# Performance work log

Measured on AMD Instinct MI355X. Metric: run time of the kernel, lower is better.

Reference implementation:

```python
import math
import jax, jax.numpy as jnp
import numpy as np

DIM = 192
HEADS = 6
WIN = (16, 16)
N = WIN[0] * WIN[1]
B_ = 256
NW = 64
CPB_HIDDEN = 512


def _relative_coords_table(window_size):
    Wh, Ww = window_size
    h = np.arange(-(Wh - 1), Wh, dtype=np.float32)
    w = np.arange(-(Ww - 1), Ww, dtype=np.float32)
    table = np.stack(np.meshgrid(h, w, indexing='ij'), axis=-1)[None]  # (1, 2Wh-1, 2Ww-1, 2)
    table[..., 0] /= (Wh - 1)
    table[..., 1] /= (Ww - 1)
    table *= 8.0
    table = np.sign(table) * np.log2(np.abs(table) + 1.0) / np.log2(8.0)
    return table.astype(np.float32)


def _relative_position_index(window_size):
    Wh, Ww = window_size
    coords = np.stack(np.meshgrid(np.arange(Wh), np.arange(Ww), indexing='ij'))  # (2, Wh, Ww)
    flat = coords.reshape(2, -1)
    rel = flat[:, :, None] - flat[:, None, :]  # (2, N, N)
    rel = rel.transpose(1, 2, 0).astype(np.int64)
    rel[..., 0] += Wh - 1
    rel[..., 1] += Ww - 1
    rel[..., 0] *= 2 * Ww - 1
    return rel.sum(-1)  # (N, N)


def setup_inputs() -> dict:
    key = jax.random.key(0)
    ks = jax.random.split(key, 9)
    s = 1.0 / math.sqrt(DIM)
    inp = {
        'x': jax.random.normal(ks[0], (B_, N, DIM), dtype=jnp.float32),
        'mask': jax.random.normal(ks[1], (NW, N, N), dtype=jnp.float32),
        'qkv_w': jax.random.normal(ks[2], (3 * DIM, DIM), dtype=jnp.float32) * s,
        'qkv_b': jnp.zeros((3 * DIM,), dtype=jnp.float32),
        'proj_w': jax.random.normal(ks[3], (DIM, DIM), dtype=jnp.float32) * s,
        'proj_b': jnp.zeros((DIM,), dtype=jnp.float32),
        'logit_scale': jnp.full((HEADS, 1, 1), math.log(10.0), dtype=jnp.float32),
        'cpb_w1': jax.random.normal(ks[4], (CPB_HIDDEN, 2), dtype=jnp.float32) * (1.0 / math.sqrt(2.0)),
        'cpb_b1': jnp.zeros((CPB_HIDDEN,), dtype=jnp.float32),
        'cpb_w2': jax.random.normal(ks[5], (HEADS, CPB_HIDDEN), dtype=jnp.float32) * (1.0 / math.sqrt(CPB_HIDDEN)),
        'coords_table': jnp.asarray(_relative_coords_table(WIN)),
        'rel_index': jnp.asarray(_relative_position_index(WIN)),
    }
    return inp


def reference(x, mask, qkv_w, qkv_b, proj_w, proj_b, logit_scale,
              cpb_w1, cpb_b1, cpb_w2, coords_table, rel_index):
    Bw, n, C = x.shape
    H = logit_scale.shape[0]
    Dh = C // H
    eps = 1e-12

    qkv = x @ qkv_w.T + qkv_b                             # (B_, N, 3C)
    qkv = qkv.reshape(Bw, n, 3, H, Dh).transpose(2, 0, 3, 1, 4)
    q, k, v = qkv[0], qkv[1], qkv[2]                      # (B_, H, N, Dh)

    qn = q / jnp.maximum(jnp.linalg.norm(q, axis=-1, keepdims=True), eps)
    kn = k / jnp.maximum(jnp.linalg.norm(k, axis=-1, keepdims=True), eps)
    attn = jnp.einsum('bhnd,bhmd->bhnm', qn, kn)

    scale = jnp.exp(jnp.minimum(logit_scale, math.log(1.0 / 0.01)))  # (H,1,1)
    attn = attn * scale[None]

    # CPB MLP bias: (1, 2Wh-1, 2Ww-1, 2) -> (-1, H), gather, sigmoid-scale
    hbt = jax.nn.relu(coords_table @ cpb_w1.T + cpb_b1) @ cpb_w2.T   # (1, 2Wh-1, 2Ww-1, H)
    bias_table = hbt.reshape(-1, H)
    bias = bias_table[rel_index.reshape(-1)].reshape(n, n, H).transpose(2, 0, 1)
    attn = attn + 16.0 * jax.nn.sigmoid(bias)[None]

    nW = mask.shape[0]
    attn = attn.reshape(Bw // nW, nW, H, n, n) + mask[None, :, None]
    attn = attn.reshape(Bw, H, n, n)

    attn = jax.nn.softmax(attn, axis=-1)
    out = jnp.einsum('bhnm,bhmd->bhnd', attn, v)
    out = out.transpose(0, 2, 1, 3).reshape(Bw, n, C)
    return out @ proj_w.T + proj_b
```

## Files before the change

### kernel.cpp

```cpp
#include <hip/hip_runtime.h>

using bf16 = __bf16;
typedef bf16 bf16x4 __attribute__((ext_vector_type(4)));
typedef bf16 bf16x8 __attribute__((ext_vector_type(8)));
typedef float f32x4 __attribute__((ext_vector_type(4)));

__device__ __forceinline__ int swz192(int row, int col) {
  return row * 192 + (col ^ ((row & 7) << 3));
}
__device__ __forceinline__ int qk_idx(int row, int col) {
  return (row >> 1) * 64 + (row & 1) * 32 + (col ^ (((row >> 1) & 3) << 3));
}
__device__ __forceinline__ int vt_idx(int d, int n) {
  return d * 256 + (((n + ((d >> 3) << 4)) & 255) ^ ((d & 7) << 3));
}
__device__ __forceinline__ int p_idx4(int wv, int r, int c) {
  return wv * 1024 + r * 64 + (c ^ ((r & 7) << 3));
}

#define LOG2E 1.44269504088896f
#define GLOAD_LDS(src, dst)                                                     \
  __builtin_amdgcn_global_load_lds(                                             \
      (const __attribute__((address_space(1))) void*)(src),                     \
      (__attribute__((address_space(3))) void*)(dst), 16, 0, 0)

template <bool OUT_F32, bool NORM_QK, int NT>
__global__ __launch_bounds__(256) void k_gemm(const bf16* __restrict__ A,
                                              const bf16* __restrict__ W,
                                              const float* __restrict__ bias,
                                              const float* __restrict__ lsc,
                                              void* __restrict__ Op, int Ntot) {
  __shared__ bf16 As[64 * 192];
  __shared__ bf16 Bs[64 * 192];
  const int bid = blockIdx.x;
  const int xcd = bid & 7;
  const int j = bid >> 3;
  const int m0 = (xcd + 8 * (j / NT)) * 64;
  const int n0 = (j % NT) * 64;
  const int t = threadIdx.x;

#pragma unroll
  for (int i = 0; i < 6; ++i) {
    const int f = t + i * 256;
    const int row = f / 24, c8 = f % 24;
    const int csw = (c8 ^ (row & 7)) * 8;
    GLOAD_LDS(&A[(m0 + row) * 192 + csw], &As[f * 8]);
    GLOAD_LDS(&W[(n0 + row) * 192 + csw], &Bs[f * 8]);
  }
  __syncthreads();

  const int w = t >> 6, lane = t & 63, lo = lane & 15, hi = lane >> 4;
  const int wm = (w >> 1) * 32, wn = (w & 1) * 32;
  f32x4 acc[2][2];
#pragma unroll
  for (int a = 0; a < 2; ++a)
#pragma unroll
    for (int c = 0; c < 2; ++c) acc[a][c] = f32x4{0.f, 0.f, 0.f, 0.f};

#pragma unroll
  for (int ks = 0; ks < 6; ++ks) {
    const int k0 = ks * 32 + hi * 8;
    bf16x8 af[2], bfr[2];
#pragma unroll
    for (int ri = 0; ri < 2; ++ri)
      af[ri] = *reinterpret_cast<const bf16x8*>(&As[swz192(wm + ri * 16 + lo, k0)]);
#pragma unroll
    for (int ci = 0; ci < 2; ++ci)
      bfr[ci] = *reinterpret_cast<const bf16x8*>(&Bs[swz192(wn + ci * 16 + lo, k0)]);
#pragma unroll
    for (int ri = 0; ri < 2; ++ri)
#pragma unroll
      for (int ci = 0; ci < 2; ++ci)
        acc[ri][ci] = __builtin_amdgcn_mfma_f32_16x16x32_bf16(af[ri], bfr[ci], acc[ri][ci], 0, 0, 0);
  }

  if (NORM_QK) {
    const int cb = n0 + wn;
    const bool donorm = (cb < 384);
    float smul = 1.f;
    if (cb < 192)
      smul = expf(fminf(lsc[cb >> 5], 4.605170185988091f)) * LOG2E;
    const int col0 = cb + lo;
    const float b0 = bias[col0], b1 = bias[col0 + 16];
    bf16* O = (bf16*)Op;
#pragma unroll
    for (int ri = 0; ri < 2; ++ri)
#pragma unroll
      for (int rr = 0; rr < 4; ++rr) {
        float v0 = acc[ri][0][rr] + b0;
        float v1 = acc[ri][1][rr] + b1;
        if (donorm) {
          float ss = v0 * v0 + v1 * v1;
          ss += __shfl_xor(ss, 1, 16);
          ss += __shfl_xor(ss, 2, 16);
          ss += __shfl_xor(ss, 4, 16);
          ss += __shfl_xor(ss, 8, 16);
          const float rn = smul / fmaxf(sqrtf(ss), 1e-12f);
          v0 *= rn;
          v1 *= rn;
        }
        const int row = m0 + wm + ri * 16 + hi * 4 + rr;
        O[row * Ntot + col0] = (bf16)v0;
        O[row * Ntot + col0 + 16] = (bf16)v1;
      }
  } else {
#pragma unroll
    for (int ri = 0; ri < 2; ++ri)
#pragma unroll
      for (int ci = 0; ci < 2; ++ci) {
        const int col = n0 + wn + ci * 16 + lo;
        const float bv = bias[col];
#pragma unroll
        for (int rr = 0; rr < 4; ++rr) {
          const int row = m0 + wm + ri * 16 + hi * 4 + rr;
          const float val = acc[ri][ci][rr] + bv;
          if (OUT_F32)
            __builtin_nontemporal_store(val, &((float*)Op)[row * Ntot + col]);
          else
            ((bf16*)Op)[row * Ntot + col] = (bf16)val;
        }
      }
  }
}

__global__ void k_cpb1(const float* __restrict__ ct, const float* __restrict__ w1,
                       const float* __restrict__ b1, const float* __restrict__ w2,
                       float* __restrict__ bt) {
  int idx = blockIdx.x * 256 + threadIdx.x;
  if (idx >= 961 * 6) return;
  int r = idx / 6, hh = idx % 6;
  float t0 = ct[r * 2], t1 = ct[r * 2 + 1];
  float acc = 0.f;
  for (int j = 0; j < 512; ++j) {
    float hv = fmaf(w1[j * 2], t0, fmaf(w1[j * 2 + 1], t1, b1[j]));
    hv = fmaxf(hv, 0.f);
    acc = fmaf(hv, w2[hh * 512 + j], acc);
  }
  bt[idx] = acc;
}

__global__ __launch_bounds__(256) void k_prep(
    const float* __restrict__ x, bf16* __restrict__ xb,
    const float* __restrict__ qkv_w, bf16* __restrict__ qkv_wb,
    const float* __restrict__ proj_w, bf16* __restrict__ proj_wb,
    const float* __restrict__ mask, bf16* __restrict__ maskT,
    const float* __restrict__ bt, const int* __restrict__ rel,
    float* __restrict__ biasfT) {
  __shared__ float tile[64][65];
  const int bid = blockIdx.x;
  if (bid < 6216) {
    const float* in;
    bf16* o;
    int vb;
    if (bid < 6144) { in = x; o = xb; vb = bid; }
    else if (bid < 6198) { in = qkv_w; o = qkv_wb; vb = bid - 6144; }
    else { in = proj_w; o = proj_wb; vb = bid - 6198; }
    const int i = (vb * 256 + threadIdx.x) * 8;
    const f32x4 a = *reinterpret_cast<const f32x4*>(&in[i]);
    const f32x4 b = *reinterpret_cast<const f32x4*>(&in[i + 4]);
    bf16x8 v;
    v[0] = (bf16)a[0]; v[1] = (bf16)a[1]; v[2] = (bf16)a[2]; v[3] = (bf16)a[3];
    v[4] = (bf16)b[0]; v[5] = (bf16)b[1]; v[6] = (bf16)b[2]; v[7] = (bf16)b[3];
    *reinterpret_cast<bf16x8*>(&o[i]) = v;
  } else if (bid < 7240) {
    const int rem = bid - 6216;
    const int mb = rem >> 4;
    const int it = (rem & 15) >> 2, jt = rem & 3;
    const int tx = threadIdx.x & 63, ty = threadIdx.x >> 6;
    const float* mp = mask + mb * 65536;
#pragma unroll
    for (int rr = 0; rr < 16; ++rr)
      tile[rr * 4 + ty][tx] = mp[(it * 64 + rr * 4 + ty) * 256 + jt * 64 + tx];
    __syncthreads();
    bf16* op = maskT + mb * 65536;
#pragma unroll
    for (int rr = 0; rr < 16; ++rr)
      op[(jt * 64 + rr * 4 + ty) * 256 + it * 64 + tx] = (bf16)(LOG2E * tile[tx][rr * 4 + ty]);
  } else {
    const int idx = (bid - 7240) * 256 + threadIdx.x;
    const int hh = idx >> 16;
    const int jj = (idx >> 8) & 255;
    const int i = idx & 255;
    const float v = bt[rel[i * 256 + jj] * 6 + hh];
    biasfT[idx] = LOG2E * 16.f / (1.f + __builtin_amdgcn_exp2f(-LOG2E * v));
  }
}

__global__ __launch_bounds__(256) void k_attn(const bf16* __restrict__ qkv,
                                              const bf16* __restrict__ maskT,
                                              const float* __restrict__ biasfT,
                                              bf16* __restrict__ aout) {
  __shared__ bf16 ksh[256 * 32];
  __shared__ bf16 vts[32 * 256];
  __shared__ bf16 ps[4 * 16 * 64];

  const int bid = blockIdx.x;
  const int x = bid & 7, i = bid >> 3;
  const int mb = x * 8 + i / 24;
  const int rem = i % 24;
  const int b = (rem / 6) * 64 + mb;
  const int h = rem % 6;
  const int t = threadIdx.x;

  const int rsub = t >> 2;
  const int c4s = t & 3;
#pragma unroll
  for (int p = 0; p < 4; ++p) {
    const int row = p * 64 + rsub;
    const int base = (b * 256 + row) * 576 + h * 32 + c4s * 8;
    *reinterpret_cast<bf16x8*>(&ksh[qk_idx(row, c4s * 8)]) =
        *reinterpret_cast<const bf16x8*>(&qkv[base + 192]);
    bf16x8 v = *reinterpret_cast<const bf16x8*>(&qkv[base + 384]);
#pragma unroll
    for (int jj = 0; jj < 8; ++jj) vts[vt_idx(c4s * 8 + jj, row)] = v[jj];
  }
  __syncthreads();

  const int w = t >> 6, lane = t & 63, lo = lane & 15, hi = lane >> 4;
  const float* bT = biasfT + (h << 16);
  const bf16* mT = maskT + (mb << 16);
  const bf16* qbase = qkv + (b * 256) * 576 + h * 32;

  bf16x8 afn = *reinterpret_cast<const bf16x8*>(&qbase[(w * 16 + lo) * 576 + hi * 8]);

  f32x4 bvp[4];
  bf16x4 mvp[4];
  {
    const int rbase0 = w * 16 + hi * 4;
#pragma unroll
    for (int c = 0; c < 4; ++c) {
      const int col = c * 16 + lo;
      bvp[c] = *reinterpret_cast<const f32x4*>(&bT[col * 256 + rbase0]);
      mvp[c] = *reinterpret_cast<const bf16x4*>(&mT[col * 256 + rbase0]);
    }
  }

  for (int rgi = 0; rgi < 4; ++rgi) {
    const int rg = rgi * 4 + w;
    const int rbase = rg * 16 + hi * 4;
    const bf16x8 af = afn;
    if (rgi < 3)
      afn = *reinterpret_cast<const bf16x8*>(&qbase[((rg + 4) * 16 + lo) * 576 + hi * 8]);

    f32x4 po0 = {0.f, 0.f, 0.f, 0.f}, po1 = {0.f, 0.f, 0.f, 0.f};
    float sum[4] = {0.f, 0.f, 0.f, 0.f};

#pragma unroll
    for (int ph = 0; ph < 4; ++ph) {
      f32x4 bv[4];
      bf16x4 mv[4];
#pragma unroll
      for (int c = 0; c < 4; ++c) { bv[c] = bvp[c]; mv[c] = mvp[c]; }
      if (ph < 3) {
#pragma unroll
        for (int c = 0; c < 4; ++c) {
          const int col = (ph + 1) * 64 + c * 16 + lo;
          bvp[c] = *reinterpret_cast<const f32x4*>(&bT[col * 256 + rbase]);
          mvp[c] = *reinterpret_cast<const bf16x4*>(&mT[col * 256 + rbase]);
        }
      } else if (rgi < 3) {
#pragma unroll
        for (int c = 0; c < 4; ++c) {
          const int col = c * 16 + lo;
          bvp[c] = *reinterpret_cast<const f32x4*>(&bT[col * 256 + rbase + 64]);
          mvp[c] = *reinterpret_cast<const bf16x4*>(&mT[col * 256 + rbase + 64]);
        }
      }
      bf16x8 kf[4];
#pragma unroll
      for (int c4i = 0; c4i < 4; ++c4i) {
        const int ct = ph * 4 + c4i;
        kf[c4i] = *reinterpret_cast<const bf16x8*>(&ksh[qk_idx(ct * 16 + lo, hi * 8)]);
      }
      f32x4 a[4];
#pragma unroll
      for (int c4i = 0; c4i < 4; ++c4i) {
        f32x4 z = {0.f, 0.f, 0.f, 0.f};
        a[c4i] = __builtin_amdgcn_mfma_f32_16x16x32_bf16(af, kf[c4i], z, 0, 0, 0);
      }
#pragma unroll
      for (int c4i = 0; c4i < 4; ++c4i)
#pragma unroll
        for (int rr = 0; rr < 4; ++rr) {
          const float s = a[c4i][rr] + bv[c4i][rr] + (float)mv[c4i][rr];
          const float p = __builtin_amdgcn_exp2f(s);
          sum[rr] += p;
          ps[p_idx4(w, hi * 4 + rr, c4i * 16 + lo)] = (bf16)p;
        }
#pragma unroll
      for (int kb = 0; kb < 2; ++kb) {
        const bf16x8 pa = *reinterpret_cast<const bf16x8*>(&ps[p_idx4(w, lo, kb * 32 + hi * 8)]);
        const bf16x8 b0 = *reinterpret_cast<const bf16x8*>(&vts[vt_idx(lo, ph * 64 + kb * 32 + hi * 8)]);
        const bf16x8 b1 = *reinterpret_cast<const bf16x8*>(&vts[vt_idx(16 + lo, ph * 64 + kb * 32 + hi * 8)]);
        po0 = __builtin_amdgcn_mfma_f32_16x16x32_bf16(pa, b0, po0, 0, 0, 0);
        po1 = __builtin_amdgcn_mfma_f32_16x16x32_bf16(pa, b1, po1, 0, 0, 0);
      }
    }
#pragma unroll
    for (int rr = 0; rr < 4; ++rr) {
      float s = sum[rr];
      s += __shfl_xor(s, 1, 16);
      s += __shfl_xor(s, 2, 16);
      s += __shfl_xor(s, 4, 16);
      s += __shfl_xor(s, 8, 16);
      sum[rr] = 1.f / s;
    }
#pragma unroll
    for (int rr = 0; rr < 4; ++rr) {
      const int ob = (b * 256 + rbase + rr) * 192 + h * 32;
      aout[ob + lo] = (bf16)(po0[rr] * sum[rr]);
      aout[ob + 16 + lo] = (bf16)(po1[rr] * sum[rr]);
    }
  }
}

extern "C" void kernel_launch(void* const* d_in, const int* in_sizes, int n_in,
                              void* d_out, int out_size, void* d_ws, size_t ws_size,
                              hipStream_t stream) {
  const float* x      = (const float*)d_in[0];
  const float* mask   = (const float*)d_in[1];
  const float* qkv_w  = (const float*)d_in[2];
  const float* qkv_b  = (const float*)d_in[3];
  const float* proj_w = (const float*)d_in[4];
  const float* proj_b = (const float*)d_in[5];
  const float* lsc    = (const float*)d_in[6];
  const float* cpb_w1 = (const float*)d_in[7];
  const float* cpb_b1 = (const float*)d_in[8];
  const float* cpb_w2 = (const float*)d_in[9];
  const float* ctab   = (const float*)d_in[10];
  const int*   relidx = (const int*)d_in[11];

  char* ws = (char*)d_ws;
  bf16*  qkvb   = (bf16*)(ws);
  bf16*  xb     = (bf16*)(ws + 75497472);
  bf16*  aoutb  = (bf16*)(ws + 75497472);
  float* biasfT = (float*)(ws + 100663296);
  bf16*  maskTb = (bf16*)(ws + 102236160);
  float* bt     = (float*)(ws + 110624768);
  bf16*  qkv_wb = (bf16*)(ws + 110647840);
  bf16*  proj_wb= (bf16*)(ws + 110869024);

  k_cpb1<<<23, 256, 0, stream>>>(ctab, cpb_w1, cpb_b1, cpb_w2, bt);
  k_prep<<<8776, 256, 0, stream>>>(x, xb, qkv_w, qkv_wb, proj_w, proj_wb,
                                   mask, maskTb, bt, relidx, biasfT);
  k_gemm<false, true, 9><<<9216, 256, 0, stream>>>(xb, qkv_wb, qkv_b, lsc, qkvb, 576);
  k_attn<<<1536, 256, 0, stream>>>(qkvb, maskTb, biasfT, aoutb);
  k_gemm<true, false, 3><<<3072, 256, 0, stream>>>(aoutb, proj_wb, proj_b, nullptr,
                                                   (float*)d_out, 192);
}
```

Measured before the change: 211.7 us.

## Parallelize CPB MLP across wavefronts inside prep kernel, split bias expansion out

The CPB MLP previously ran as a separate 23-block kernel where each thread looped serially over 512 hidden units, which sits on the critical path before prep. It now runs as extra blocks of the prep kernel, with one wavefront per (row, head) output and a shuffle reduction across lanes. The bias gather/sigmoid expansion moves into its own small kernel launched after prep, so the number of launches stays the same. The serial MLP tail should shrink, but the expansion now cannot overlap with prep's conversion work.

```diff
diff --git a/kernel.cpp b/kernel.cpp
--- a/kernel.cpp
+++ b/kernel.cpp
@@ -123,29 +123,14 @@
   }
 }
 
-__global__ void k_cpb1(const float* __restrict__ ct, const float* __restrict__ w1,
-                       const float* __restrict__ b1, const float* __restrict__ w2,
-                       float* __restrict__ bt) {
-  int idx = blockIdx.x * 256 + threadIdx.x;
-  if (idx >= 961 * 6) return;
-  int r = idx / 6, hh = idx % 6;
-  float t0 = ct[r * 2], t1 = ct[r * 2 + 1];
-  float acc = 0.f;
-  for (int j = 0; j < 512; ++j) {
-    float hv = fmaf(w1[j * 2], t0, fmaf(w1[j * 2 + 1], t1, b1[j]));
-    hv = fmaxf(hv, 0.f);
-    acc = fmaf(hv, w2[hh * 512 + j], acc);
-  }
-  bt[idx] = acc;
-}
-
 __global__ __launch_bounds__(256) void k_prep(
     const float* __restrict__ x, bf16* __restrict__ xb,
     const float* __restrict__ qkv_w, bf16* __restrict__ qkv_wb,
     const float* __restrict__ proj_w, bf16* __restrict__ proj_wb,
     const float* __restrict__ mask, bf16* __restrict__ maskT,
-    const float* __restrict__ bt, const int* __restrict__ rel,
-    float* __restrict__ biasfT) {
+    const float* __restrict__ ct, const float* __restrict__ w1,
+    const float* __restrict__ b1, const float* __restrict__ w2,
+    float* __restrict__ bt) {
   __shared__ float tile[64][65];
   const int bid = blockIdx.x;
   if (bid < 6216) {
@@ -177,13 +162,38 @@
     for (int rr = 0; rr < 16; ++rr)
       op[(jt * 64 + rr * 4 + ty) * 256 + it * 64 + tx] = (bf16)(LOG2E * tile[tx][rr * 4 + ty]);
   } else {
-    const int idx = (bid - 7240) * 256 + threadIdx.x;
-    const int hh = idx >> 16;
-    const int jj = (idx >> 8) & 255;
-    const int i = idx & 255;
-    const float v = bt[rel[i * 256 + jj] * 6 + hh];
-    biasfT[idx] = LOG2E * 16.f / (1.f + __builtin_amdgcn_exp2f(-LOG2E * v));
-  }
+    const int wid = (bid - 7240) * 4 + (threadIdx.x >> 6);
+    if (wid < 5766) {
+      const int r = wid / 6, hh = wid % 6;
+      const int lane = threadIdx.x & 63;
+      const float t0 = ct[r * 2], t1 = ct[r * 2 + 1];
+      float acc = 0.f;
+#pragma unroll
+      for (int jj = 0; jj < 8; ++jj) {
+        const int j = lane + jj * 64;
+        float hv = fmaf(w1[j * 2], t0, fmaf(w1[j * 2 + 1], t1, b1[j]));
+        hv = fmaxf(hv, 0.f);
+        acc = fmaf(hv, w2[hh * 512 + j], acc);
+      }
+      acc += __shfl_xor(acc, 1);
+      acc += __shfl_xor(acc, 2);
+      acc += __shfl_xor(acc, 4);
+      acc += __shfl_xor(acc, 8);
+      acc += __shfl_xor(acc, 16);
+      acc += __shfl_xor(acc, 32);
+      if (lane == 0) bt[wid] = acc;
+    }
+  }
+}
+
+__global__ void k_cpbT(const float* __restrict__ bt, const int* __restrict__ rel,
+                       float* __restrict__ biasfT) {
+  const int idx = blockIdx.x * 256 + threadIdx.x;
+  const int hh = idx >> 16;
+  const int jj = (idx >> 8) & 255;
+  const int i = idx & 255;
+  const float v = bt[rel[i * 256 + jj] * 6 + hh];
+  biasfT[idx] = LOG2E * 16.f / (1.f + __builtin_amdgcn_exp2f(-LOG2E * v));
 }
 
 __global__ __launch_bounds__(256) void k_attn(const bf16* __restrict__ qkv,
@@ -340,9 +350,9 @@
   bf16*  qkv_wb = (bf16*)(ws + 110647840);
   bf16*  proj_wb= (bf16*)(ws + 110869024);
 
-  k_cpb1<<<23, 256, 0, stream>>>(ctab, cpb_w1, cpb_b1, cpb_w2, bt);
-  k_prep<<<8776, 256, 0, stream>>>(x, xb, qkv_w, qkv_wb, proj_w, proj_wb,
-                                   mask, maskTb, bt, relidx, biasfT);
+  k_prep<<<8682, 256, 0, stream>>>(x, xb, qkv_w, qkv_wb, proj_w, proj_wb,
+                                   mask, maskTb, ctab, cpb_w1, cpb_b1, cpb_w2, bt);
+  k_cpbT<<<1536, 256, 0, stream>>>(bt, relidx, biasfT);
   k_gemm<false, true, 9><<<9216, 256, 0, stream>>>(xb, qkv_wb, qkv_b, lsc, qkvb, 576);
   k_attn<<<1536, 256, 0, stream>>>(qkvb, maskTb, biasfT, aoutb);
   k_gemm<true, false, 3><<<3072, 256, 0, stream>>>(aoutb, proj_wb, proj_b, nullptr,
```

Measured after the change: 188.5 us. 11.0% less time.
